# Performance work log

Hardware: AMD Instinct MI355X
Metric: run time of the kernel (lower is better)

The kernel has to match this reference:

```python
import jax, jax.numpy as jnp
import numpy as np

N_LEAVES = 4096
NF = N_LEAVES            # one-hot leaf feature dim
NN = 2 * N_LEAVES - 1    # nodes in binary backbone tree
HID = 512
T_MIN, T_MAX = 0.0, 1.0  # time_grid endpoints


def _belief_prop(node_sample, ch0, ch1, parent):
    """Postorder c/d recursion then preorder correction, as in node_embedding_site_backbone.
    Node ids are topologically ordered (children < parent), so postorder = 0..NN-1."""
    is_leaf = node_sample >= 0
    leaf_d = jax.nn.one_hot(jnp.clip(node_sample, 0), NF, dtype=jnp.float32)
    c0 = jnp.zeros((NN,), jnp.float32)
    d0 = jnp.zeros((NN, NF), jnp.float32)

    def post(carry, u):
        c, d = carry
        cc = c[ch0[u]] + c[ch1[u]]
        dd = d[ch0[u]] + d[ch1[u]]
        cu = 1.0 / (3.0 - cc)
        du = cu * dd
        cu = jnp.where(is_leaf[u], 0.0, cu)
        du = jnp.where(is_leaf[u], leaf_d[u], du)
        return (c.at[u].set(cu), d.at[u].set(du)), None

    (c, d), _ = jax.lax.scan(post, (c0, d0), jnp.arange(NN))
    root = NN - 1

    def pre(d, u):
        du = jnp.where(u == root, d[u], c[u] * d[parent[u]] + d[u])
        return d.at[u].set(du), None

    d, _ = jax.lax.scan(pre, d, jnp.arange(NN - 1, -1, -1))
    return d


def _gcn_layer(x, neigh, W, b):
    # neighbor-list GCN: mean over {self} U valid neighbors, then linear
    n = x.shape[0]
    safe = jnp.where(neigh < 0, n, neigh)  # -1 -> extra zero row
    x_ext = jnp.concatenate([x, jnp.zeros((1, x.shape[1]), x.dtype)], axis=0)
    deg = 1.0 + jnp.sum(neigh >= 0, axis=1).astype(x.dtype)
    agg = (x + x_ext[safe].sum(axis=1)) / deg[:, None]
    return agg @ W + b


def setup_inputs():
    rng = np.random.default_rng(0)
    ch0 = -np.ones(NN, np.int64)
    ch1 = -np.ones(NN, np.int64)
    parent = -np.ones(NN, np.int64)
    avail = list(range(N_LEAVES))
    for u in range(N_LEAVES, NN):  # random binary coalescent topology
        a = avail.pop(int(rng.integers(len(avail))))
        b = avail.pop(int(rng.integers(len(avail))))
        ch0[u], ch1[u] = a, b
        parent[a] = u
        parent[b] = u
        avail.append(u)
    root = NN - 1
    node_sample = np.where(np.arange(NN) < N_LEAVES, np.arange(NN), -1).astype(np.int64)
    neigh = -np.ones((NN + 1, 3), np.int64)
    for u in range(NN):
        if u == root:
            neigh[u] = [ch0[u], ch1[u], -1]
        else:
            neigh[u] = [parent[u], ch0[u], ch1[u]]
    branch_child = np.arange(NN, dtype=np.int64)
    is_root = (branch_child == root).astype(np.float32)

    key = jax.random.key(0)
    ks = jax.random.split(key, 8)
    w = lambda k, s: jax.random.normal(k, s, jnp.float32) * 0.02
    E = 4 * HID + 2
    return {
        "node_sample": jnp.asarray(node_sample),
        "ch0": jnp.asarray(ch0),
        "ch1": jnp.asarray(ch1),
        "parent": jnp.asarray(parent),
        "neigh": jnp.asarray(neigh),
        "branch_child": jnp.asarray(branch_child),
        "current_focal_leaf": 7,
        "time_value": jax.random.uniform(ks[0], (NN,), jnp.float32),
        "is_root": jnp.asarray(is_root),
        "W_gnn1": w(ks[1], (NF, HID)), "b_gnn1": jnp.zeros((HID,), jnp.float32),
        "W_gnn2": w(ks[2], (HID, HID)), "b_gnn2": jnp.zeros((HID,), jnp.float32),
        "W_h1": w(ks[3], (E, HID)), "b_h1": jnp.zeros((HID,), jnp.float32),
        "W_h2": w(ks[4], (HID, HID)), "b_h2": jnp.zeros((HID,), jnp.float32),
        "W_h3": w(ks[5], (HID, 1)), "b_h3": jnp.zeros((1,), jnp.float32),
    }


def reference(node_sample, ch0, ch1, parent, neigh, branch_child, current_focal_leaf,
              time_value, is_root, W_gnn1, b_gnn1, W_gnn2, b_gnn2,
              W_h1, b_h1, W_h2, b_h2, W_h3, b_h3):
    d = _belief_prop(node_sample, ch0, ch1, parent)                  # (NN, NF)
    focal_feat = jax.nn.one_hot(current_focal_leaf, NF, dtype=jnp.float32)
    x = jnp.concatenate([d, focal_feat[None, :]], axis=0)            # (NN+1, NF)

    h = jax.nn.relu(_gcn_layer(x, neigh, W_gnn1, b_gnn1))
    emb = _gcn_layer(h, neigh, W_gnn2, b_gnn2)                       # (NN+1, HID)

    h_focal = emb[NN]                                                # appended focal node
    h_tgt = emb[branch_child]                                        # (A, HID)
    h_f = jnp.broadcast_to(h_focal[None, :], h_tgt.shape)
    t_norm = (time_value - T_MIN) / (T_MAX - T_MIN + 1e-8)
    ef = jnp.concatenate([h_f, h_tgt, jnp.abs(h_f - h_tgt), h_f * h_tgt,
                          t_norm[:, None], is_root[:, None]], axis=-1)  # (A, 4*HID+2)

    z = jax.nn.elu(ef @ W_h1 + b_h1)
    z = jax.nn.elu(z @ W_h2 + b_h2)
    logits = (z @ W_h3 + b_h3)[:, 0]
    probs = jax.nn.softmax(logits, axis=0)
    return logits, probs, ef, emb, focal_feat
```

## Files before the change

kernel.cpp:

```cpp
#include <hip/hip_runtime.h>
#include <hip/hip_bf16.h>
#include <math.h>

#define NNODES 8191
#define ROOT   8190
#define NROWS  8192
#define FOCALR 8191
#define NLEAF  4096
#define HID    512
#define EDIM   2050

#define OUT_LOGITS 0
#define OUT_PROBS  8191
#define OUT_EF     16382
#define OUT_EMB    16807932
#define OUT_FOCAL  21002236

typedef float  f32x4 __attribute__((ext_vector_type(4)));
typedef float  f32x2 __attribute__((ext_vector_type(2)));
typedef float  floatx4 __attribute__((ext_vector_type(4)));
typedef short  short8 __attribute__((ext_vector_type(8)));
typedef unsigned short u16;
typedef unsigned short u16x8 __attribute__((ext_vector_type(8)));
typedef unsigned short u16x4 __attribute__((ext_vector_type(4)));

__device__ __forceinline__ f32x4 ldg4(const float* p) { return *(const f32x4*)p; }
__device__ __forceinline__ f32x2 ldg2(const float* p) { return *(const f32x2*)p; }
__device__ __forceinline__ void stg4(float* p, f32x4 v) { *(f32x4*)p = v; }

__device__ __forceinline__ void st_row(float* p, f32x4 v0, f32x4 v1) {
    asm volatile("global_store_dwordx4 %0, %1, off sc0 sc1\n\t"
                 "global_store_dwordx4 %0, %2, off offset:1024 sc0 sc1"
                 :: "v"(p), "v"(v0), "v"(v1) : "memory");
}
__device__ __forceinline__ void st_flag_ordered(float* p, float v) {
    asm volatile("s_waitcnt vmcnt(0)\n\tglobal_store_dword %0, %1, off sc0 sc1"
                 :: "v"(p), "v"(v) : "memory");
}
__device__ __forceinline__ void spin1(const float* pc, float& cv) {
    for (;;) {
        asm volatile("global_load_dword %0, %1, off sc0 sc1\n\ts_waitcnt vmcnt(0)"
                     : "=&v"(cv) : "v"(pc) : "memory");
        if (cv > 0.0f) break;
        __builtin_amdgcn_s_sleep(1);
    }
}
__device__ __forceinline__ void spin2(const float* pa, const float* pb,
                                      float& va, float& vb) {
    for (;;) {
        asm volatile("global_load_dword %0, %2, off sc0 sc1\n\t"
                     "global_load_dword %1, %3, off sc0 sc1\n\t"
                     "s_waitcnt vmcnt(0)"
                     : "=&v"(va), "=&v"(vb) : "v"(pa), "v"(pb) : "memory");
        if (va > 0.0f && vb > 0.0f) break;
        __builtin_amdgcn_s_sleep(1);
    }
}
__device__ __forceinline__ void spin3(const float* pa, const float* pb,
                                      const float* pc, float& va, float& vb, float& vc) {
    for (;;) {
        asm volatile("global_load_dword %0, %3, off sc0 sc1\n\t"
                     "global_load_dword %1, %4, off sc0 sc1\n\t"
                     "global_load_dword %2, %5, off sc0 sc1\n\t"
                     "s_waitcnt vmcnt(0)"
                     : "=&v"(va), "=&v"(vb), "=&v"(vc)
                     : "v"(pa), "v"(pb), "v"(pc) : "memory");
        if (va > 0.0f && vb > 0.0f && vc > 0.0f) break;
        __builtin_amdgcn_s_sleep(1);
    }
}
__device__ __forceinline__ void spin4(const float* p0, const float* p1,
                                      const float* p2, const float* p3,
                                      float& v0, float& v1, float& v2, float& v3) {
    for (;;) {
        asm volatile("global_load_dword %0, %4, off sc0 sc1\n\t"
                     "global_load_dword %1, %5, off sc0 sc1\n\t"
                     "global_load_dword %2, %6, off sc0 sc1\n\t"
                     "global_load_dword %3, %7, off sc0 sc1\n\t"
                     "s_waitcnt vmcnt(0)"
                     : "=&v"(v0), "=&v"(v1), "=&v"(v2), "=&v"(v3)
                     : "v"(p0), "v"(p1), "v"(p2), "v"(p3) : "memory");
        if (v0 > 0.0f && v1 > 0.0f && v2 > 0.0f && v3 > 0.0f) break;
        __builtin_amdgcn_s_sleep(1);
    }
}
__device__ __forceinline__ void rows1_cv(const float* p, f32x4& a0, f32x4& a1) {
    asm volatile("global_load_dwordx4 %0, %2, off sc0 sc1\n\t"
                 "global_load_dwordx4 %1, %2, off offset:1024 sc0 sc1\n\t"
                 "s_waitcnt vmcnt(0)"
                 : "=&v"(a0), "=&v"(a1) : "v"(p) : "memory");
}
__device__ __forceinline__ void rows2_cv(const float* p0, const float* p1,
                                         f32x4& a0, f32x4& a1, f32x4& b0, f32x4& b1) {
    asm volatile("global_load_dwordx4 %0, %4, off sc0 sc1\n\t"
                 "global_load_dwordx4 %1, %4, off offset:1024 sc0 sc1\n\t"
                 "global_load_dwordx4 %2, %5, off sc0 sc1\n\t"
                 "global_load_dwordx4 %3, %5, off offset:1024 sc0 sc1\n\t"
                 "s_waitcnt vmcnt(0)"
                 : "=&v"(a0), "=&v"(a1), "=&v"(b0), "=&v"(b1)
                 : "v"(p0), "v"(p1) : "memory");
}
__device__ __forceinline__ void rows3_cv(const float* p0, const float* p1,
                                         const float* p2,
                                         f32x4& a0, f32x4& a1, f32x4& b0, f32x4& b1,
                                         f32x4& c0, f32x4& c1) {
    asm volatile("global_load_dwordx4 %0, %6, off sc0 sc1\n\t"
                 "global_load_dwordx4 %1, %6, off offset:1024 sc0 sc1\n\t"
                 "global_load_dwordx4 %2, %7, off sc0 sc1\n\t"
                 "global_load_dwordx4 %3, %7, off offset:1024 sc0 sc1\n\t"
                 "global_load_dwordx4 %4, %8, off sc0 sc1\n\t"
                 "global_load_dwordx4 %5, %8, off offset:1024 sc0 sc1\n\t"
                 "s_waitcnt vmcnt(0)"
                 : "=&v"(a0), "=&v"(a1), "=&v"(b0), "=&v"(b1), "=&v"(c0), "=&v"(c1)
                 : "v"(p0), "v"(p1), "v"(p2) : "memory");
}
__device__ __forceinline__ void rows4_cv(const float* p0, const float* p1,
                                         const float* p2, const float* p3,
                                         f32x4& a0, f32x4& a1, f32x4& b0, f32x4& b1,
                                         f32x4& c0, f32x4& c1, f32x4& d0, f32x4& d1) {
    asm volatile("global_load_dwordx4 %0, %8, off sc0 sc1\n\t"
                 "global_load_dwordx4 %1, %8, off offset:1024 sc0 sc1\n\t"
                 "global_load_dwordx4 %2, %9, off sc0 sc1\n\t"
                 "global_load_dwordx4 %3, %9, off offset:1024 sc0 sc1\n\t"
                 "global_load_dwordx4 %4, %10, off sc0 sc1\n\t"
                 "global_load_dwordx4 %5, %10, off offset:1024 sc0 sc1\n\t"
                 "global_load_dwordx4 %6, %11, off sc0 sc1\n\t"
                 "global_load_dwordx4 %7, %11, off offset:1024 sc0 sc1\n\t"
                 "s_waitcnt vmcnt(0)"
                 : "=&v"(a0), "=&v"(a1), "=&v"(b0), "=&v"(b1),
                   "=&v"(c0), "=&v"(c1), "=&v"(d0), "=&v"(d1)
                 : "v"(p0), "v"(p1), "v"(p2), "v"(p3) : "memory");
}
__device__ __forceinline__ f32x4 fma4(f32x4 s, float cv, f32x4 pv) { return s + cv * pv; }

__device__ __forceinline__ u16 f2bf(float x) {
    union { float f; unsigned u; } u; u.f = x;
    unsigned r = u.u + 0x7fffu + ((u.u >> 16) & 1u);
    return (u16)(r >> 16);
}
__device__ __forceinline__ float b2f(u16 h) {
    union { unsigned u; float f; } x; x.u = ((unsigned)h) << 16; return x.f;
}

__global__ __launch_bounds__(256) void stage1_kernel(const int* __restrict__ ns,
                                                     const int* __restrict__ ch0,
                                                     const int* __restrict__ ch1,
                                                     const int* __restrict__ par,
                                                     const float* __restrict__ W1,
                                                     float* __restrict__ c,
                                                     float* __restrict__ ypost,
                                                     float* __restrict__ y,
                                                     float* __restrict__ flag2,
                                                     const float* __restrict__ W2,
                                                     const float* __restrict__ Wh2,
                                                     const float* __restrict__ Wh1,
                                                     u16* __restrict__ wte,
                                                     u16* __restrict__ wt2,
                                                     u16* __restrict__ WTz1,
                                                     const int* __restrict__ cfl,
                                                     float* __restrict__ outf,
                                                     const float* __restrict__ bh1,
                                                     float* __restrict__ bprime,
                                                     const float* __restrict__ bh3,
                                                     float* __restrict__ outlog) {
    __shared__ float tile[32][33];
    int bid = blockIdx.x, tid = threadIdx.x;

    if (bid < 256) {
        int gtid = bid * 256 + tid;
        int wave = gtid >> 6, lane = gtid & 63;
        int j0 = lane * 4;

        for (int u = NLEAF + wave; u < NNODES; u += 1024) {
            int a = ch0[u], b = ch1[u];
            int la = ns[a], lb = ns[b];
            const float *ra0, *ra1, *rb0, *rb1;
            int ga0 = -1, ga1 = -1, gb0 = -1, gb1 = -1;
            if (la >= 0) { ra0 = W1 + (long)la * HID; ra1 = ra0; }
            else {
                int x0 = ch0[a], x1 = ch1[a];
                int n0 = ns[x0], n1 = ns[x1];
                if (n0 >= 0) ra0 = W1 + (long)n0 * HID;
                else { ra0 = ypost + (long)x0 * HID; ga0 = x0; }
                if (n1 >= 0) ra1 = W1 + (long)n1 * HID;
                else { ra1 = ypost + (long)x1 * HID; ga1 = x1; }
            }
            if (lb >= 0) { rb0 = W1 + (long)lb * HID; rb1 = rb0; }
            else {
                int x0 = ch0[b], x1 = ch1[b];
                int n0 = ns[x0], n1 = ns[x1];
                if (n0 >= 0) rb0 = W1 + (long)n0 * HID;
                else { rb0 = ypost + (long)x0 * HID; gb0 = x0; }
                if (n1 >= 0) rb1 = W1 + (long)n1 * HID;
                else { rb1 = ypost + (long)x1 * HID; gb1 = x1; }
            }
            float ca0 = 0.f, ca1 = 0.f, cb0 = 0.f, cb1 = 0.f;
            if ((ga0 | ga1 | gb0 | gb1) >= 0) {
                int w0 = ga0 >= 0 ? ga0 : ga1 >= 0 ? ga1 : gb0 >= 0 ? gb0 : gb1;
                float s0, s1, s2, s3;
                spin4(c + (ga0 >= 0 ? ga0 : w0), c + (ga1 >= 0 ? ga1 : w0),
                      c + (gb0 >= 0 ? gb0 : w0), c + (gb1 >= 0 ? gb1 : w0),
                      s0, s1, s2, s3);
                if (ga0 >= 0) ca0 = s0;
                if (ga1 >= 0) ca1 = s1;
                if (gb0 >= 0) cb0 = s2;
                if (gb1 >= 0) cb1 = s3;
            }
            f32x4 qa00, qa01, qa10, qa11, qb00, qb01, qb10, qb11;
            rows4_cv(ra0 + j0, ra1 + j0, rb0 + j0, rb1 + j0,
                     qa00, qa01, qa10, qa11, qb00, qb01, qb10, qb11);
            f32x4 A0, A1, B0, B1; float cA, cB;
            if (la >= 0) { cA = 0.0f; A0 = qa00; A1 = qa01; }
            else {
                cA = 1.0f / (3.0f - (ca0 + ca1));
                A0 = (qa00 + qa10) * cA; A1 = (qa01 + qa11) * cA;
            }
            if (lb >= 0) { cB = 0.0f; B0 = qb00; B1 = qb01; }
            else {
                cB = 1.0f / (3.0f - (cb0 + cb1));
                B0 = (qb00 + qb10) * cB; B1 = (qb01 + qb11) * cB;
            }
            float cu = 1.0f / (3.0f - (cA + cB));
            st_row(ypost + (long)u * HID + j0, (A0 + B0) * cu, (A1 + B1) * cu);
            if (lane == 0) st_flag_ordered(&c[u], cu);
        }

        for (int u = ROOT - wave; u >= NLEAF; u -= 1024) {
            float* dst = y + (long)u * HID + j0;
            if (u == ROOT) {
                float cr;
                spin1(c + ROOT, cr);
                f32x4 s0, s1;
                rows1_cv(ypost + (long)ROOT * HID + j0, s0, s1);
                st_row(dst, s0, s1);
            } else {
                int p = par[u];
                if (p == ROOT) {
                    float cr, cu;
                    spin2(c + ROOT, c + u, cr, cu);
                    f32x4 s0, s1, r0, r1;
                    rows2_cv(ypost + (long)u * HID + j0, ypost + (long)ROOT * HID + j0,
                             s0, s1, r0, r1);
                    st_row(dst, fma4(s0, cu, r0), fma4(s1, cu, r1));
                } else {
                    int gp = par[p];
                    float f2, cu, cp;
                    spin3(flag2 + gp, c + u, c + p, f2, cu, cp);
                    f32x4 s0, s1, pp0, pp1, gg0, gg1;
                    rows3_cv(ypost + (long)u * HID + j0, ypost + (long)p * HID + j0,
                             y + (long)gp * HID + j0, s0, s1, pp0, pp1, gg0, gg1);
                    f32x4 yp0 = fma4(pp0, cp, gg0);
                    f32x4 yp1 = fma4(pp1, cp, gg1);
                    st_row(dst, fma4(s0, cu, yp0), fma4(s1, cu, yp1));
                }
            }
            if (lane == 0) st_flag_ordered(&flag2[u], 1.0f);
        }
        return;
    }

    if (bid < 1024) {
        int t = bid - 256;
        int bx = t & 15, by = t >> 4;
        int sec = by >> 4, kt = by & 15;
        int tx = tid & 31, ty = tid >> 5;
        int n0 = bx * 32, k0 = kt * 32;
        const float* src = (sec == 0) ? W2 : (sec == 1) ? Wh2 : (Wh1 + (long)1024 * HID);
        u16* dst = (sec == 0) ? wte : (sec == 1) ? wt2 : WTz1;
        int ld = (sec == 2) ? 1024 : 512;
        int koff = (sec == 2) ? 512 : 0;
#pragma unroll
        for (int i = 0; i < 4; i++)
            tile[ty + i * 8][tx] = src[(long)(k0 + ty + i * 8) * HID + n0 + tx];
        __syncthreads();
#pragma unroll
        for (int i = 0; i < 4; i++)
            dst[(long)(n0 + ty + i * 8) * ld + koff + k0 + tx] = f2bf(tile[tx][ty + i * 8]);
        return;
    }

    int cf = cfl[0];
    for (int i = tid; i < NLEAF; i += 256) outf[i] = (i == cf) ? 1.0f : 0.0f;
    float b3v = bh3[0];
    for (int i = tid; i < NNODES; i += 256) outlog[i] = b3v;
    for (int i = tid; i < 512; i += 256) bprime[i] = bh1[i];
}

__global__ __launch_bounds__(256) void emb_fan_kernel(const float* __restrict__ emb,
                                                      const float* __restrict__ Wh1,
                                                      u16* __restrict__ WTz1,
                                                      float* __restrict__ bprime) {
    __shared__ float tB[32][33];
    __shared__ float tD[32][33];
    int bid = blockIdx.x, tid = threadIdx.x;
    const float* hf = emb + (long)FOCALR * HID;

    if (bid < 256) {
        int tx = tid & 31, ty = tid >> 5;
        int n0 = (bid & 15) * 32, k0 = (bid >> 4) * 32;
#pragma unroll
        for (int i = 0; i < 4; i++) {
            tB[ty + i * 8][tx] = Wh1[(long)(512 + k0 + ty + i * 8) * HID + n0 + tx];
            tD[ty + i * 8][tx] = Wh1[(long)(1536 + k0 + ty + i * 8) * HID + n0 + tx];
        }
        __syncthreads();
#pragma unroll
        for (int i = 0; i < 4; i++) {
            float hfk = hf[k0 + tx];
            WTz1[(long)(n0 + ty + i * 8) * 1024 + k0 + tx] =
                f2bf(tB[tx][ty + i * 8] + hfk * tD[tx][ty + i * 8]);
        }
        return;
    }
    int kc = bid - 256;
    float s0 = 0.0f, s1 = 0.0f;
#pragma unroll 4
    for (int k = kc * 64; k < kc * 64 + 64; k++) {
        float h = hf[k];
        s0 += h * Wh1[(long)k * HID + tid];
        s1 += h * Wh1[(long)k * HID + 256 + tid];
    }
    atomicAdd(bprime + tid, s0);
    atomicAdd(bprime + 256 + tid, s1);
}

__global__ __launch_bounds__(128) void gcn_agg_kernel(const float* __restrict__ xinf,
                                                      const int* __restrict__ neigh,
                                                      const float* __restrict__ bias,
                                                      const int* __restrict__ ns,
                                                      const int* __restrict__ cfl,
                                                      const float* __restrict__ W1,
                                                      u16* __restrict__ xoutb) {
    int u = blockIdx.x;
    int t = threadIdx.x;
    int n0 = neigh[u * 3 + 0], n1 = neigh[u * 3 + 1], n2 = neigh[u * 3 + 2];
    float deg = 1.0f + (n0 >= 0) + (n1 >= 0) + (n2 >= 0);
    auto rowp = [&](int v) -> const float* {
        if (v == FOCALR) return W1 + (long)cfl[0] * HID;
        int nv = ns[v];
        return (nv >= 0) ? (W1 + (long)nv * HID) : (xinf + (long)v * HID);
    };
    f32x4 s = ldg4(rowp(u) + t * 4);
    if (n0 >= 0) s += ldg4(rowp(n0) + t * 4);
    if (n1 >= 0) s += ldg4(rowp(n1) + t * 4);
    if (n2 >= 0) s += ldg4(rowp(n2) + t * 4);
    s *= (1.0f / deg);
    s += ldg4(bias + t * 4);
    s.x = fmaxf(s.x, 0.f); s.y = fmaxf(s.y, 0.f); s.z = fmaxf(s.z, 0.f); s.w = fmaxf(s.w, 0.f);
    u16x4 h; h[0] = f2bf(s.x); h[1] = f2bf(s.y); h[2] = f2bf(s.z); h[3] = f2bf(s.w);
    *(u16x4*)(xoutb + (long)u * HID + t * 4) = h;
}

__device__ __forceinline__ int sw_idx(int row, int kc8) {
    return (row * 8 + (kc8 ^ (row & 7))) * 8;
}

template <int ACT, int AGEN, int LOG, int AGG, int EF>
__global__ __launch_bounds__(256, 3) void gemm_v5(const u16* __restrict__ Abf,
                                                  const u16* __restrict__ WT,
                                                  const float* __restrict__ bias,
                                                  const int* __restrict__ bc,
                                                  const float* __restrict__ tv,
                                                  const float* __restrict__ isr,
                                                  const float* __restrict__ Wtail,
                                                  float* __restrict__ Cf,
                                                  u16* __restrict__ Cbf,
                                                  int M, int K,
                                                  const float* __restrict__ W3,
                                                  float* __restrict__ outlog,
                                                  const int* __restrict__ neigh,
                                                  const float* __restrict__ embf,
                                                  float* __restrict__ efout) {
    __shared__ u16 As[2][64 * 64];
    __shared__ u16 Ws[2][128 * 64];
    if (EF && blockIdx.x >= 512) {
        int eb = blockIdx.x - 512;
        int u = eb * 2 + (threadIdx.x >> 7);
        int t = threadIdx.x & 127;
        if (u < NNODES) {
            const float* hfp = embf + (long)FOCALR * HID;
            const float* ht = embf + (long)bc[u] * HID;
            f32x4 f = ldg4(hfp + 4 * t);
            f32x4 h = ldg4(ht + 4 * t);
            float* row = efout + (long)u * EDIM;
            *(f32x4*)(row + 4 * t) = f;
            *(f32x4*)(row + 512 + 4 * t) = h;
            f32x4 d;
            d.x = fabsf(f.x - h.x); d.y = fabsf(f.y - h.y);
            d.z = fabsf(f.z - h.z); d.w = fabsf(f.w - h.w);
            *(f32x4*)(row + 1024 + 4 * t) = d;
            *(f32x4*)(row + 1536 + 4 * t) = f * h;
            if (t == 0) {
                row[2048] = tv[u];
                row[2049] = isr[u];
            }
        }
        return;
    }
    const int tid = threadIdx.x, lane = tid & 63;
    const int wm = (tid >> 6) >> 1, wn = (tid >> 6) & 1;
    const int bid1 = blockIdx.x;
    const int bn = (bid1 & 3) * 128, bm = (bid1 >> 2) * 64;
    const int kq = lane >> 4, lr = lane & 15;
    const int srow = tid >> 3, schunk = tid & 7;
    const int nk = K >> 6;
    floatx4 acc[2][4] = {};

    int btc[2];
    if (AGEN) {
#pragma unroll
        for (int i = 0; i < 2; i++) {
            int gr = bm + srow + i * 32;
            btc[i] = bc[gr < M ? gr : 0];
        }
    }
    int nbr[2][3];
    float invdeg[2];
    if (AGG) {
#pragma unroll
        for (int i = 0; i < 2; i++) {
            int gr = bm + srow + i * 32;
            int v0 = neigh[gr * 3 + 0], v1 = neigh[gr * 3 + 1], v2 = neigh[gr * 3 + 2];
            nbr[i][0] = v0; nbr[i][1] = v1; nbr[i][2] = v2;
            invdeg[i] = 1.0f / (1.0f + (v0 >= 0) + (v1 >= 0) + (v2 >= 0));
        }
    }

    u16x8 pf_hf, pf_a[2], pf_b[4], pf_n[2][3];

    auto prefetch = [&](int kk) {
        if (AGEN) {
            int cb = (kk & 7) * 64 + schunk * 8;
            pf_hf = *(const u16x8*)(Abf + (long)FOCALR * HID + cb);
#pragma unroll
            for (int i = 0; i < 2; i++)
                pf_a[i] = *(const u16x8*)(Abf + (long)btc[i] * HID + cb);
        } else if (AGG) {
            long kof = (long)(kk * 64 + schunk * 8);
#pragma unroll
            for (int i = 0; i < 2; i++) {
                int gr = bm + srow + i * 32;
                pf_a[i] = *(const u16x8*)(Abf + (long)gr * HID + kof);
#pragma unroll
                for (int k = 0; k < 3; k++)
                    pf_n[i][k] = (nbr[i][k] >= 0)
                        ? *(const u16x8*)(Abf + (long)nbr[i][k] * HID + kof)
                        : (u16x8){0, 0, 0, 0, 0, 0, 0, 0};
            }
        } else {
            long kof = (long)(kk * 64 + schunk * 8);
#pragma unroll
            for (int i = 0; i < 2; i++) {
                int gr = bm + srow + i * 32;
                if (gr < M) pf_a[i] = *(const u16x8*)(Abf + (long)gr * K + kof);
                else        pf_a[i] = (u16x8){0,0,0,0,0,0,0,0};
            }
        }
#pragma unroll
        for (int i = 0; i < 4; i++)
            pf_b[i] = *(const u16x8*)(WT + (long)(bn + srow + i * 32) * K + kk * 64 + schunk * 8);
    };

    auto commit = [&](int kk, int buf) {
        if (AGEN) {
            int sec = kk >> 3;
#pragma unroll
            for (int i = 0; i < 2; i++) {
                u16x8 v;
                if (sec == 0) v = pf_a[i];
                else {
#pragma unroll
                    for (int q = 0; q < 8; q++) v[q] = f2bf(fabsf(b2f(pf_hf[q]) - b2f(pf_a[i][q])));
                }
                if (bm + srow + i * 32 >= M) v = (u16x8){0,0,0,0,0,0,0,0};
                *(u16x8*)&As[buf][sw_idx(srow + i * 32, schunk)] = v;
            }
        } else if (AGG) {
#pragma unroll
            for (int i = 0; i < 2; i++) {
                u16x8 v;
#pragma unroll
                for (int q = 0; q < 8; q++) {
                    float s = b2f(pf_a[i][q]);
                    s += b2f(pf_n[i][0][q]);
                    s += b2f(pf_n[i][1][q]);
                    s += b2f(pf_n[i][2][q]);
                    v[q] = f2bf(s * invdeg[i]);
                }
                *(u16x8*)&As[buf][sw_idx(srow + i * 32, schunk)] = v;
            }
        } else {
#pragma unroll
            for (int i = 0; i < 2; i++)
                *(u16x8*)&As[buf][sw_idx(srow + i * 32, schunk)] = pf_a[i];
        }
#pragma unroll
        for (int i = 0; i < 4; i++)
            *(u16x8*)&Ws[buf][sw_idx(srow + i * 32, schunk)] = pf_b[i];
    };

    prefetch(0);
    commit(0, 0);
    __syncthreads();

    for (int kk = 0; kk < nk; kk++) {
        int cur = kk & 1;
        bool more = (kk + 1) < nk;
        if (more) prefetch(kk + 1);
#pragma unroll
        for (int kc = 0; kc < 2; kc++) {
            short8 af[2], bf8[4];
#pragma unroll
            for (int t2 = 0; t2 < 2; t2++)
                af[t2]  = *(short8*)&As[cur][sw_idx(wm * 32 + t2 * 16 + lr, kc * 4 + kq)];
#pragma unroll
            for (int t2 = 0; t2 < 4; t2++)
                bf8[t2] = *(short8*)&Ws[cur][sw_idx(wn * 64 + t2 * 16 + lr, kc * 4 + kq)];
#pragma unroll
            for (int i2 = 0; i2 < 2; i2++)
#pragma unroll
                for (int j = 0; j < 4; j++)
                    acc[i2][j] = __builtin_amdgcn_mfma_f32_16x16x32_bf16(af[i2], bf8[j], acc[i2][j], 0, 0, 0);
        }
        if (more) {
            __syncthreads();
            commit(kk + 1, cur ^ 1);
            __syncthreads();
        }
    }

    float lsum[2][4] = {};
    float w3v[4] = {};
    if (LOG) {
#pragma unroll
        for (int j = 0; j < 4; j++) w3v[j] = W3[bn + wn * 64 + j * 16 + lr];
    }
#pragma unroll
    for (int i = 0; i < 2; i++) {
        int row0 = bm + wm * 32 + i * 16 + kq * 4;
#pragma unroll
        for (int j = 0; j < 4; j++) {
            int col = bn + wn * 64 + j * 16 + lr;
            float bv = bias[col];
            float t0 = 0.f, t1 = 0.f;
            if (AGEN) { t0 = Wtail[col]; t1 = Wtail[512 + col]; }
#pragma unroll
            for (int r = 0; r < 4; r++) {
                int gr = row0 + r;
                if (gr < M) {
                    float v = acc[i][j][r] + bv;
                    if (AGEN) v += tv[gr] * t0 + isr[gr] * t1;
                    if (ACT == 2) v = (v > 0.0f) ? v : (expf(v) - 1.0f);
                    if (LOG) lsum[i][r] += v * w3v[j];
                    if (Cf)  Cf[(long)gr * HID + col] = v;
                    if (Cbf) Cbf[(long)gr * HID + col] = f2bf(v);
                }
            }
        }
    }
    if (LOG) {
#pragma unroll
        for (int i = 0; i < 2; i++) {
            int row0 = bm + wm * 32 + i * 16 + kq * 4;
#pragma unroll
            for (int r = 0; r < 4; r++) {
                float s = lsum[i][r];
                s += __shfl_xor(s, 1);
                s += __shfl_xor(s, 2);
                s += __shfl_xor(s, 4);
                s += __shfl_xor(s, 8);
                if (lr == 0) {
                    int gr = row0 + r;
                    if (gr < M) atomicAdd(outlog + gr, s);
                }
            }
        }
    }
}

__global__ __launch_bounds__(1024) void softmax_kernel(const float* __restrict__ lg,
                                                       float* __restrict__ probs) {
    __shared__ float red[16];
    __shared__ float gmax_s, gsum_s;
    int t = threadIdx.x, wid = t >> 6, lane = t & 63;
    float m = -3.4e38f;
    for (int i = t; i < NNODES; i += 1024) m = fmaxf(m, lg[i]);
    for (int o = 32; o; o >>= 1) m = fmaxf(m, __shfl_down(m, o));
    if (lane == 0) red[wid] = m;
    __syncthreads();
    if (t == 0) {
        float g = red[0];
        for (int i = 1; i < 16; i++) g = fmaxf(g, red[i]);
        gmax_s = g;
    }
    __syncthreads();
    float gmax = gmax_s;
    float s = 0.0f;
    for (int i = t; i < NNODES; i += 1024) s += expf(lg[i] - gmax);
    for (int o = 32; o; o >>= 1) s += __shfl_down(s, o);
    if (lane == 0) red[wid] = s;
    __syncthreads();
    if (t == 0) {
        float g = 0.0f;
        for (int i = 0; i < 16; i++) g += red[i];
        gsum_s = g;
    }
    __syncthreads();
    float inv = 1.0f / gsum_s;
    for (int i = t; i < NNODES; i += 1024) probs[i] = expf(lg[i] - gmax) * inv;
}

extern "C" void kernel_launch(void* const* d_in, const int* in_sizes, int n_in,
                              void* d_out, int out_size, void* d_ws, size_t ws_size,
                              hipStream_t stream) {
    const int*   ns    = (const int*)d_in[0];
    const int*   ch0   = (const int*)d_in[1];
    const int*   ch1   = (const int*)d_in[2];
    const int*   par   = (const int*)d_in[3];
    const int*   neigh = (const int*)d_in[4];
    const int*   bc    = (const int*)d_in[5];
    const int*   cfl   = (const int*)d_in[6];
    const float* tv    = (const float*)d_in[7];
    const float* isr   = (const float*)d_in[8];
    const float* W1    = (const float*)d_in[9];
    const float* b1    = (const float*)d_in[10];
    const float* W2    = (const float*)d_in[11];
    const float* b2    = (const float*)d_in[12];
    const float* Wh1   = (const float*)d_in[13];
    const float* bh1   = (const float*)d_in[14];
    const float* Wh2   = (const float*)d_in[15];
    const float* bh2   = (const float*)d_in[16];
    const float* Wh3   = (const float*)d_in[17];
    const float* bh3   = (const float*)d_in[18];

    float* out = (float*)d_out;
    float* out_logits = out + OUT_LOGITS;
    float* out_probs  = out + OUT_PROBS;
    float* out_ef     = out + OUT_EF;
    float* out_emb    = out + OUT_EMB;
    float* out_focal  = out + OUT_FOCAL;

    const size_t MB = 1024 * 1024;
    char* ws = (char*)d_ws;
    float* c      = (float*)(ws);
    float* flag2  = (float*)(ws + 40960);
    float* buf0   = (float*)(ws + 81920);
    float* buf1   = (float*)(ws + 81920 + 16 * MB);
    float* buf2   = (float*)(ws + 81920 + 32 * MB);
    u16*   wte    = (u16*)  (ws + 81920 + 48 * MB);
    u16*   wt2    = (u16*)  (ws + 81920 + 48 * MB + 512 * 1024);
    u16*   wtz1   = (u16*)  (ws + 81920 + 49 * MB);
    float* bprime = (float*)(ws + 81920 + 50 * MB);

    float* ypost  = buf0;
    float* y      = buf1;
    u16*   emb_bf = (u16*)((char*)buf1 + 8 * MB);
    u16*   h_bf   = (u16*)buf2;
    u16*   z1_bf  = (u16*)buf2;

    stage1_kernel<<<dim3(1025), dim3(256), 0, stream>>>(ns, ch0, ch1, par, W1, c, ypost,
                                                        y, flag2, W2, Wh2, Wh1, wte, wt2,
                                                        wtz1, cfl, out_focal, bh1, bprime,
                                                        bh3, out_logits);
    gcn_agg_kernel<<<dim3(NROWS), dim3(128), 0, stream>>>(y, neigh, b1, ns, cfl, W1, h_bf);
    gemm_v5<0, 0, 0, 1, 0><<<dim3(512), dim3(256), 0, stream>>>(
        h_bf, wte, b2, nullptr, nullptr, nullptr, nullptr, out_emb, emb_bf,
        NROWS, HID, nullptr, nullptr, neigh, nullptr, nullptr);
    emb_fan_kernel<<<dim3(264), dim3(256), 0, stream>>>(out_emb, Wh1, wtz1, bprime);
    gemm_v5<2, 1, 0, 0, 1><<<dim3(4608), dim3(256), 0, stream>>>(
        emb_bf, wtz1, bprime, bc, tv, isr, Wh1 + (long)2048 * HID, nullptr, z1_bf,
        NNODES, 1024, nullptr, nullptr, nullptr, out_emb, out_ef);
    gemm_v5<2, 0, 1, 0, 0><<<dim3(512), dim3(256), 0, stream>>>(
        z1_bf, wt2, bh2, nullptr, nullptr, nullptr, nullptr, nullptr, nullptr,
        NNODES, HID, Wh3, out_logits, nullptr, nullptr, nullptr);
    softmax_kernel<<<dim3(1), dim3(1024), 0, stream>>>(out_logits, out_probs);
}
```

Measured before the change: 265.5 us.

## Fuse focal-row fan-out into second GCN GEMM via flag-based cross-block sync

Removes the separate emb_fan_kernel launch. Its work now runs in extra blocks (512..775) of the second GCN GEMM, which spin on per-column-tile flags. The GEMM blocks that own the last row tile write the focal embedding row to a scratch buffer with coherent stores, then raise those flags. This saves one kernel launch and its tail gap and lets the fan-out overlap the GEMM tail. The risk is spin-wait deadlock if the consumer blocks occupy slots before the producer tiles are scheduled, and the wasted spin time.

```diff
diff --git a/kernel.cpp b/kernel.cpp
--- a/kernel.cpp
+++ b/kernel.cpp
@@ -33,9 +33,16 @@
                  "global_store_dwordx4 %0, %2, off offset:1024 sc0 sc1"
                  :: "v"(p), "v"(v0), "v"(v1) : "memory");
 }
+__device__ __forceinline__ void st_wt1(float* p, float v) {
+    asm volatile("global_store_dword %0, %1, off sc0 sc1" :: "v"(p), "v"(v) : "memory");
+}
 __device__ __forceinline__ void st_flag_ordered(float* p, float v) {
     asm volatile("s_waitcnt vmcnt(0)\n\tglobal_store_dword %0, %1, off sc0 sc1"
                  :: "v"(p), "v"(v) : "memory");
+}
+__device__ __forceinline__ void ld1_sc(const float* p, float& v) {
+    asm volatile("global_load_dword %0, %1, off sc0 sc1\n\ts_waitcnt vmcnt(0)"
+                 : "=&v"(v) : "v"(p) : "memory");
 }
 __device__ __forceinline__ void spin1(const float* pc, float& cv) {
     for (;;) {
@@ -162,7 +169,8 @@
                                                      const float* __restrict__ bh1,
                                                      float* __restrict__ bprime,
                                                      const float* __restrict__ bh3,
-                                                     float* __restrict__ outlog) {
+                                                     float* __restrict__ outlog,
+                                                     float* __restrict__ hfflag) {
     __shared__ float tile[32][33];
     int bid = blockIdx.x, tid = threadIdx.x;
 
@@ -284,44 +292,7 @@
     float b3v = bh3[0];
     for (int i = tid; i < NNODES; i += 256) outlog[i] = b3v;
     for (int i = tid; i < 512; i += 256) bprime[i] = bh1[i];
-}
-
-__global__ __launch_bounds__(256) void emb_fan_kernel(const float* __restrict__ emb,
-                                                      const float* __restrict__ Wh1,
-                                                      u16* __restrict__ WTz1,
-                                                      float* __restrict__ bprime) {
-    __shared__ float tB[32][33];
-    __shared__ float tD[32][33];
-    int bid = blockIdx.x, tid = threadIdx.x;
-    const float* hf = emb + (long)FOCALR * HID;
-
-    if (bid < 256) {
-        int tx = tid & 31, ty = tid >> 5;
-        int n0 = (bid & 15) * 32, k0 = (bid >> 4) * 32;
-#pragma unroll
-        for (int i = 0; i < 4; i++) {
-            tB[ty + i * 8][tx] = Wh1[(long)(512 + k0 + ty + i * 8) * HID + n0 + tx];
-            tD[ty + i * 8][tx] = Wh1[(long)(1536 + k0 + ty + i * 8) * HID + n0 + tx];
-        }
-        __syncthreads();
-#pragma unroll
-        for (int i = 0; i < 4; i++) {
-            float hfk = hf[k0 + tx];
-            WTz1[(long)(n0 + ty + i * 8) * 1024 + k0 + tx] =
-                f2bf(tB[tx][ty + i * 8] + hfk * tD[tx][ty + i * 8]);
-        }
-        return;
-    }
-    int kc = bid - 256;
-    float s0 = 0.0f, s1 = 0.0f;
-#pragma unroll 4
-    for (int k = kc * 64; k < kc * 64 + 64; k++) {
-        float h = hf[k];
-        s0 += h * Wh1[(long)k * HID + tid];
-        s1 += h * Wh1[(long)k * HID + 256 + tid];
-    }
-    atomicAdd(bprime + tid, s0);
-    atomicAdd(bprime + 256 + tid, s1);
+    if (tid < 4) hfflag[tid] = 0.0f;
 }
 
 __global__ __launch_bounds__(128) void gcn_agg_kernel(const float* __restrict__ xinf,
@@ -355,7 +326,7 @@
     return (row * 8 + (kc8 ^ (row & 7))) * 8;
 }
 
-template <int ACT, int AGEN, int LOG, int AGG, int EF>
+template <int ACT, int AGEN, int LOG, int AGG, int EF, int PUBFAN>
 __global__ __launch_bounds__(256, 3) void gemm_v5(const u16* __restrict__ Abf,
                                                   const u16* __restrict__ WT,
                                                   const float* __restrict__ bias,
@@ -370,7 +341,12 @@
                                                   float* __restrict__ outlog,
                                                   const int* __restrict__ neigh,
                                                   const float* __restrict__ embf,
-                                                  float* __restrict__ efout) {
+                                                  float* __restrict__ efout,
+                                                  const float* __restrict__ Wh1,
+                                                  u16* __restrict__ WTz1,
+                                                  float* __restrict__ bprime,
+                                                  float* __restrict__ hfsc,
+                                                  float* __restrict__ hfflag) {
     __shared__ u16 As[2][64 * 64];
     __shared__ u16 Ws[2][128 * 64];
     if (EF && blockIdx.x >= 512) {
@@ -397,6 +373,50 @@
         }
         return;
     }
+    if (PUBFAN && blockIdx.x >= 512) {
+        int fb = blockIdx.x - 512;
+        int tid = threadIdx.x;
+        float g0, g1, g2, g3;
+        spin4(hfflag, hfflag + 1, hfflag + 2, hfflag + 3, g0, g1, g2, g3);
+        float* tBf = (float*)&As[0][0];
+        float* tDf = tBf + 32 * 33;
+        if (fb < 256) {
+            int tx = tid & 31, ty = tid >> 5;
+            int n0 = (fb & 15) * 32, k0 = (fb >> 4) * 32;
+            float hfk;
+            ld1_sc(hfsc + k0 + tx, hfk);
+#pragma unroll
+            for (int i = 0; i < 4; i++) {
+                tBf[(ty + i * 8) * 33 + tx] = Wh1[(long)(512 + k0 + ty + i * 8) * HID + n0 + tx];
+                tDf[(ty + i * 8) * 33 + tx] = Wh1[(long)(1536 + k0 + ty + i * 8) * HID + n0 + tx];
+            }
+            __syncthreads();
+#pragma unroll
+            for (int i = 0; i < 4; i++) {
+                WTz1[(long)(n0 + ty + i * 8) * 1024 + k0 + tx] =
+                    f2bf(tBf[tx * 33 + ty + i * 8] + hfk * tDf[tx * 33 + ty + i * 8]);
+            }
+        } else {
+            int kc = fb - 256;
+            if (tid < 64) {
+                float v;
+                ld1_sc(hfsc + kc * 64 + tid, v);
+                tBf[tid] = v;
+            }
+            __syncthreads();
+            float s0 = 0.0f, s1 = 0.0f;
+#pragma unroll 4
+            for (int k2 = 0; k2 < 64; k2++) {
+                float h = tBf[k2];
+                int k = kc * 64 + k2;
+                s0 += h * Wh1[(long)k * HID + tid];
+                s1 += h * Wh1[(long)k * HID + 256 + tid];
+            }
+            atomicAdd(bprime + tid, s0);
+            atomicAdd(bprime + 256 + tid, s1);
+        }
+        return;
+    }
     const int tid = threadIdx.x, lane = tid & 63;
     const int wm = (tid >> 6) >> 1, wn = (tid >> 6) & 1;
     const int bid1 = blockIdx.x;
@@ -554,6 +574,7 @@
                     if (LOG) lsum[i][r] += v * w3v[j];
                     if (Cf)  Cf[(long)gr * HID + col] = v;
                     if (Cbf) Cbf[(long)gr * HID + col] = f2bf(v);
+                    if (PUBFAN && gr == FOCALR) st_wt1(hfsc + col, v);
                 }
             }
         }
@@ -575,6 +596,11 @@
                 }
             }
         }
+    }
+    if (PUBFAN && bm == 8128) {
+        asm volatile("s_waitcnt vmcnt(0)" ::: "memory");
+        __syncthreads();
+        if (tid == 0) st_wt1(hfflag + (bn >> 7), 1.0f);
     }
 }
 
@@ -651,6 +677,8 @@
     u16*   wt2    = (u16*)  (ws + 81920 + 48 * MB + 512 * 1024);
     u16*   wtz1   = (u16*)  (ws + 81920 + 49 * MB);
     float* bprime = (float*)(ws + 81920 + 50 * MB);
+    float* hfsc   = (float*)(ws + 81920 + 50 * MB + 4096);
+    float* hfflag = (float*)(ws + 81920 + 50 * MB + 8192);
 
     float* ypost  = buf0;
     float* y      = buf1;
@@ -661,17 +689,19 @@
     stage1_kernel<<<dim3(1025), dim3(256), 0, stream>>>(ns, ch0, ch1, par, W1, c, ypost,
                                                         y, flag2, W2, Wh2, Wh1, wte, wt2,
                                                         wtz1, cfl, out_focal, bh1, bprime,
-                                                        bh3, out_logits);
+                                                        bh3, out_logits, hfflag);
     gcn_agg_kernel<<<dim3(NROWS), dim3(128), 0, stream>>>(y, neigh, b1, ns, cfl, W1, h_bf);
-    gemm_v5<0, 0, 0, 1, 0><<<dim3(512), dim3(256), 0, stream>>>(
+    gemm_v5<0, 0, 0, 1, 0, 1><<<dim3(776), dim3(256), 0, stream>>>(
         h_bf, wte, b2, nullptr, nullptr, nullptr, nullptr, out_emb, emb_bf,
-        NROWS, HID, nullptr, nullptr, neigh, nullptr, nullptr);
-    emb_fan_kernel<<<dim3(264), dim3(256), 0, stream>>>(out_emb, Wh1, wtz1, bprime);
-    gemm_v5<2, 1, 0, 0, 1><<<dim3(4608), dim3(256), 0, stream>>>(
+        NROWS, HID, nullptr, nullptr, neigh, nullptr, nullptr,
+        Wh1, wtz1, bprime, hfsc, hfflag);
+    gemm_v5<2, 1, 0, 0, 1, 0><<<dim3(4608), dim3(256), 0, stream>>>(
         emb_bf, wtz1, bprime, bc, tv, isr, Wh1 + (long)2048 * HID, nullptr, z1_bf,
-        NNODES, 1024, nullptr, nullptr, nullptr, out_emb, out_ef);
-    gemm_v5<2, 0, 1, 0, 0><<<dim3(512), dim3(256), 0, stream>>>(
+        NNODES, 1024, nullptr, nullptr, nullptr, out_emb, out_ef,
+        nullptr, nullptr, nullptr, nullptr, nullptr);
+    gemm_v5<2, 0, 1, 0, 0, 0><<<dim3(512), dim3(256), 0, stream>>>(
         z1_bf, wt2, bh2, nullptr, nullptr, nullptr, nullptr, nullptr, nullptr,
-        NNODES, HID, Wh3, out_logits, nullptr, nullptr, nullptr);
+        NNODES, HID, Wh3, out_logits, nullptr, nullptr, nullptr,
+        nullptr, nullptr, nullptr, nullptr, nullptr);
     softmax_kernel<<<dim3(1), dim3(1024), 0, stream>>>(out_logits, out_probs);
 }
```

New measurement: 270.9 us. +2.0%, slower.
